# Optimization experiments

Measured on AMD Instinct MI355X. Metric: run time of the kernel, lower is better.

Reference implementation:

```python
import jax, jax.numpy as jnp
import numpy as np

NH = 16   # num_heads
HD = 128  # head_dim
HS = 2048 # hidden_size
LI, LT = 2048, 512
MLP = 4 * HS


def _ln(x, s, b):
    m = jnp.mean(x, axis=-1, keepdims=True)
    v = jnp.var(x, axis=-1, keepdims=True)
    return (x - m) * jax.lax.rsqrt(v + 1e-6) * s + b


def _rms(x, s):
    return x * jax.lax.rsqrt(jnp.mean(x * x, axis=-1, keepdims=True) + 1e-6) * s


def _mod6(vec, w, b):
    a = (jax.nn.silu(vec) @ w + b)[:, None, :]
    return jnp.split(a, 6, axis=-1)  # shift1,scale1,gate1,shift2,scale2,gate2


def _rope(x, pe):
    B, H, L, D = x.shape
    xr = x.reshape(B, H, L, D // 2, 1, 2)
    return (pe[..., 0] * xr[..., 0] + pe[..., 1] * xr[..., 1]).reshape(B, H, L, D)


def _attention(q, k, v, pe):
    q = _rope(q, pe)
    k = _rope(k, pe)
    scores = jnp.einsum('bhqd,bhkd->bhqk', q, k) * (q.shape[-1] ** -0.5)
    p = jax.nn.softmax(scores, axis=-1)
    o = jnp.einsum('bhqk,bhkd->bhqd', p, v)
    B, H, L, D = o.shape
    return o.transpose(0, 2, 1, 3).reshape(B, L, H * D)


def _prenorm_qkv(x, shift, scale, ln_s, ln_b, qkv_w, qkv_b, qn, kn):
    xm = (1.0 + scale) * _ln(x, ln_s, ln_b) + shift
    y = xm @ qkv_w + qkv_b
    B, L, _ = y.shape
    y = y.reshape(B, L, 3, NH, HD).transpose(2, 0, 3, 1, 4)  # K B H L D
    q, k, v = y[0], y[1], y[2]
    return _rms(q, qn), _rms(k, kn), v


def _forward(img, txt, vec, pe,
             img_mod_w, img_mod_b, img_norm1_s, img_norm1_b, img_qkv_w, img_qkv_b,
             img_qn_s, img_kn_s, img_proj_w, img_proj_b, img_norm2_s, img_norm2_b,
             img_mlp_w1, img_mlp_b1, img_mlp_w2, img_mlp_b2,
             txt_mod_w, txt_mod_b, txt_norm1_s, txt_norm1_b, txt_qkv_w, txt_qkv_b,
             txt_qn_s, txt_kn_s, txt_proj_w, txt_proj_b, txt_norm2_s, txt_norm2_b,
             txt_mlp_w1, txt_mlp_b1, txt_mlp_w2, txt_mlp_b2):
    i_sh1, i_sc1, i_g1, i_sh2, i_sc2, i_g2 = _mod6(vec, img_mod_w, img_mod_b)
    t_sh1, t_sc1, t_g1, t_sh2, t_sc2, t_g2 = _mod6(vec, txt_mod_w, txt_mod_b)

    iq, ik, iv = _prenorm_qkv(img, i_sh1, i_sc1, img_norm1_s, img_norm1_b,
                              img_qkv_w, img_qkv_b, img_qn_s, img_kn_s)
    tq, tk, tv = _prenorm_qkv(txt, t_sh1, t_sc1, txt_norm1_s, txt_norm1_b,
                              txt_qkv_w, txt_qkv_b, txt_qn_s, txt_kn_s)

    q = jnp.concatenate((tq, iq), axis=2)
    k = jnp.concatenate((tk, ik), axis=2)
    v = jnp.concatenate((tv, iv), axis=2)
    attn = _attention(q, k, v, pe)  # [B, LT+LI, HS]
    Lt = txt.shape[1]
    txt_attn, img_attn = attn[:, :Lt], attn[:, Lt:]

    img = img + i_g1 * (img_attn @ img_proj_w + img_proj_b)
    img_h = (1.0 + i_sc2) * _ln(img, img_norm2_s, img_norm2_b) + i_sh2
    img = img + i_g2 * (jax.nn.gelu(img_h @ img_mlp_w1 + img_mlp_b1) @ img_mlp_w2 + img_mlp_b2)

    txt = txt + t_g1 * (txt_attn @ txt_proj_w + txt_proj_b)
    txt_h = (1.0 + t_sc2) * _ln(txt, txt_norm2_s, txt_norm2_b) + t_sh2
    txt = txt + t_g2 * (jax.nn.gelu(txt_h @ txt_mlp_w1 + txt_mlp_b1) @ txt_mlp_w2 + txt_mlp_b2)
    return img, txt


def setup_inputs() -> dict:
    key = jax.random.key(0)
    ki = iter(jax.random.split(key, 48))
    def n(shape, s=0.02):
        return jax.random.normal(next(ki), shape, jnp.float32) * s
    d = {
        'img': jax.random.normal(next(ki), (1, LI, HS), jnp.float32),
        'txt': jax.random.normal(next(ki), (1, LT, HS), jnp.float32),
        'vec': jax.random.normal(next(ki), (1, HS), jnp.float32),
        'pe': jax.random.normal(next(ki), (1, 1, LT + LI, HD // 2, 2, 2), jnp.float32),
    }
    for p in ('img', 'txt'):
        d[p + '_mod_w'] = n((HS, 6 * HS)); d[p + '_mod_b'] = jnp.zeros((6 * HS,), jnp.float32)
        d[p + '_norm1_s'] = jnp.ones((HS,), jnp.float32); d[p + '_norm1_b'] = jnp.zeros((HS,), jnp.float32)
        d[p + '_qkv_w'] = n((HS, 3 * HS)); d[p + '_qkv_b'] = jnp.zeros((3 * HS,), jnp.float32)
        d[p + '_qn_s'] = jnp.ones((HD,), jnp.float32); d[p + '_kn_s'] = jnp.ones((HD,), jnp.float32)
        d[p + '_proj_w'] = n((HS, HS)); d[p + '_proj_b'] = jnp.zeros((HS,), jnp.float32)
        d[p + '_norm2_s'] = jnp.ones((HS,), jnp.float32); d[p + '_norm2_b'] = jnp.zeros((HS,), jnp.float32)
        d[p + '_mlp_w1'] = n((HS, MLP)); d[p + '_mlp_b1'] = jnp.zeros((MLP,), jnp.float32)
        d[p + '_mlp_w2'] = n((MLP, HS)); d[p + '_mlp_b2'] = jnp.zeros((HS,), jnp.float32)
    return d


def reference(img, txt, vec, pe,
              img_mod_w, img_mod_b, img_norm1_s, img_norm1_b, img_qkv_w, img_qkv_b,
              img_qn_s, img_kn_s, img_proj_w, img_proj_b, img_norm2_s, img_norm2_b,
              img_mlp_w1, img_mlp_b1, img_mlp_w2, img_mlp_b2,
              txt_mod_w, txt_mod_b, txt_norm1_s, txt_norm1_b, txt_qkv_w, txt_qkv_b,
              txt_qn_s, txt_kn_s, txt_proj_w, txt_proj_b, txt_norm2_s, txt_norm2_b,
              txt_mlp_w1, txt_mlp_b1, txt_mlp_w2, txt_mlp_b2):
    return _forward(img, txt, vec, pe,
                    img_mod_w, img_mod_b, img_norm1_s, img_norm1_b, img_qkv_w, img_qkv_b,
                    img_qn_s, img_kn_s, img_proj_w, img_proj_b, img_norm2_s, img_norm2_b,
                    img_mlp_w1, img_mlp_b1, img_mlp_w2, img_mlp_b2,
                    txt_mod_w, txt_mod_b, txt_norm1_s, txt_norm1_b, txt_qkv_w, txt_qkv_b,
                    txt_qn_s, txt_kn_s, txt_proj_w, txt_proj_b, txt_norm2_s, txt_norm2_b,
                    txt_mlp_w1, txt_mlp_b1, txt_mlp_w2, txt_mlp_b2)
```

## Files before the change

kernel.cpp:

```cpp
#include <hip/hip_runtime.h>
#include <hip/hip_bf16.h>
#include <math.h>

typedef __bf16 bf16;
typedef __bf16 bf16x2 __attribute__((ext_vector_type(2)));
typedef __bf16 bf16x4 __attribute__((ext_vector_type(4)));
typedef __bf16 bf16x8 __attribute__((ext_vector_type(8)));
typedef float f32x4 __attribute__((ext_vector_type(4)));

#define HS 2048
#define NH 16
#define HD 128
#define LT 512
#define LI 2048
#define LQ 2560
#define MLP_D 8192
#define SPLIT 4
#define KVS (LQ / SPLIT)
#define KVBLK 32
#define NTILES (KVS / KVBLK)

__device__ __forceinline__ f32x4 mfma16(bf16x8 a, bf16x8 b, f32x4 c) {
  return __builtin_amdgcn_mfma_f32_16x16x32_bf16(a, b, c, 0, 0, 0);
}

__device__ __forceinline__ void gl_lds16(const bf16* g, bf16* l) {
  __builtin_amdgcn_global_load_lds((const __attribute__((address_space(1))) void*)g,
                                   (__attribute__((address_space(3))) void*)l, 16, 0, 0);
}

__global__ void k_silu(const float* __restrict__ v, float* __restrict__ s) {
  int i = blockIdx.x * 256 + threadIdx.x;
  float x = v[i];
  s[i] = x / (1.f + expf(-x));
}

__global__ __launch_bounds__(256) void k_mod_partial(
    const float* __restrict__ s, const float* __restrict__ w_txt,
    const float* __restrict__ w_img, float* __restrict__ part) {
  int strm = blockIdx.x / 48;
  int n = (blockIdx.x % 48) * 256 + threadIdx.x;
  const float* w = strm ? w_img : w_txt;
  int k0 = blockIdx.y * 256;
  __shared__ float sl[256];
  sl[threadIdx.x] = s[k0 + threadIdx.x];
  __syncthreads();
  float acc = 0.f;
  for (int k = 0; k < 256; k++)
    acc += sl[k] * w[(size_t)(k0 + k) * 12288 + n];
  part[((size_t)blockIdx.y * 2 + strm) * 12288 + n] = acc;
}

__global__ __launch_bounds__(256) void k_mod_reduce(
    const float* __restrict__ part, const float* __restrict__ b_txt,
    const float* __restrict__ b_img, float* __restrict__ mod) {
  int strm = blockIdx.x / 48;
  int n = (blockIdx.x % 48) * 256 + threadIdx.x;
  float acc = strm ? b_img[n] : b_txt[n];
  for (int kc = 0; kc < 8; kc++)
    acc += part[((size_t)kc * 2 + strm) * 12288 + n];
  mod[(size_t)strm * 12288 + n] = acc;
}

__global__ __launch_bounds__(256) void k_transpose_cvt(
    const float* __restrict__ src, bf16* __restrict__ dst, int R, int C) {
  __shared__ float t[64][65];
  int tx = threadIdx.x & 63, ty = threadIdx.x >> 6;
  int c0 = blockIdx.x * 64, r0 = blockIdx.y * 64;
  for (int i = 0; i < 64; i += 4)
    t[ty + i][tx] = src[(size_t)(r0 + ty + i) * C + c0 + tx];
  __syncthreads();
#pragma unroll
  for (int j = 0; j < 2; j++) {
    int c = (threadIdx.x >> 3) + j * 32;
    int gg = (threadIdx.x & 7) * 8;
    bf16x8 ov;
#pragma unroll
    for (int k = 0; k < 8; k++) ov[k] = (bf16)t[gg + k][c];
    *(bf16x8*)(dst + (size_t)(c0 + c) * R + r0 + gg) = ov;
  }
}

__global__ __launch_bounds__(256) void k_ln_mod(
    const float* __restrict__ x0, const float* __restrict__ x1,
    const float* __restrict__ ls0, const float* __restrict__ lb0,
    const float* __restrict__ ls1, const float* __restrict__ lb1,
    const float* __restrict__ mod0, const float* __restrict__ mod1,
    int shidx, int scidx, bf16* __restrict__ out) {
  int r = blockIdx.x;
  int strm = r >= LT;
  const float* x = strm ? (x1 + (size_t)(r - LT) * HS) : (x0 + (size_t)r * HS);
  const float* ls = strm ? ls1 : ls0;
  const float* lb = strm ? lb1 : lb0;
  const float* md = strm ? mod1 : mod0;
  const float* sh = md + (size_t)shidx * HS;
  const float* sc = md + (size_t)scidx * HS;
  int t = threadIdx.x;
  float4 a = ((const float4*)x)[t * 2];
  float4 b = ((const float4*)x)[t * 2 + 1];
  float xv[8] = {a.x, a.y, a.z, a.w, b.x, b.y, b.z, b.w};
  float sum = 0.f, sq = 0.f;
#pragma unroll
  for (int j = 0; j < 8; j++) { sum += xv[j]; sq += xv[j] * xv[j]; }
#pragma unroll
  for (int m = 32; m; m >>= 1) { sum += __shfl_xor(sum, m); sq += __shfl_xor(sq, m); }
  __shared__ float red[8];
  int lane = t & 63, wid = t >> 6;
  if (!lane) { red[wid] = sum; red[wid + 4] = sq; }
  __syncthreads();
  float ts = red[0] + red[1] + red[2] + red[3];
  float tq = red[4] + red[5] + red[6] + red[7];
  float mean = ts * (1.f / HS);
  float var = tq * (1.f / HS) - mean * mean;
  float inv = rsqrtf(var + 1e-6f);
  int c0 = t * 8;
  bf16x8 ov;
#pragma unroll
  for (int j = 0; j < 8; j++) {
    int c = c0 + j;
    float v = ((xv[j] - mean) * inv * ls[c] + lb[c]) * (1.f + sc[c]) + sh[c];
    ov[j] = (bf16)v;
  }
  *(bf16x8*)(out + (size_t)r * HS + c0) = ov;
}

template <int MODE>
__global__ __launch_bounds__(512, 2) void k_gemm256(
    const bf16* __restrict__ A, int K, int N, int Ksz,
    const bf16* __restrict__ BT0, const bf16* __restrict__ BT1,
    const float* __restrict__ bias0, const float* __restrict__ bias1,
    void* __restrict__ out0, void* __restrict__ out1) {
  __shared__ bf16 As[2][128 * 64];
  __shared__ bf16 Bs[2][256 * 64];
  int tid = threadIdx.x;
  int bn = blockIdx.x, bm = blockIdx.y;
  int strm = (bm * 128) >= LT;
  int lm = bm * 128 - strm * LT;
  const bf16* BT = strm ? BT1 : BT0;
  int lane = tid & 63, wid = tid >> 6;
  int wr = wid >> 2, wc = wid & 3;
  int srow = tid >> 3;
  int col8 = (((tid & 7) ^ (srow & 7)) << 3);
  const bf16* Ag = A + (size_t)(bm * 128 + srow) * K + col8;
  const bf16* Bg = BT + (size_t)(bn * 256 + srow) * K + col8;
  int kbeg = MODE == 4 ? blockIdx.z * Ksz : 0;
  int nk = Ksz / 64;
  auto stage = [&](int buf, int kt) {
    int k0 = kbeg + kt * 64;
#pragma unroll
    for (int j = 0; j < 2; j++)
      gl_lds16(Ag + (size_t)(j * 64) * K + k0, &As[buf][j * 4096 + tid * 8]);
#pragma unroll
    for (int j = 0; j < 4; j++)
      gl_lds16(Bg + (size_t)(j * 64) * K + k0, &Bs[buf][j * 4096 + tid * 8]);
  };
  f32x4 acc[4][4] = {};
  int r16 = lane & 15, g = lane >> 4;
  int sa = r16 & 7;
  stage(0, 0);
  int cur = 0;
  for (int kt = 0; kt < nk; kt++) {
    __syncthreads();
    if (kt + 1 < nk) stage(cur ^ 1, kt + 1);
    bf16x8 af[4][2], bfr[4][2];
#pragma unroll
    for (int m = 0; m < 4; m++) {
      int ar = wr * 64 + m * 16 + r16;
#pragma unroll
      for (int kk = 0; kk < 2; kk++)
        af[m][kk] = *(const bf16x8*)&As[cur][ar * 64 + (((kk * 4 + g) ^ sa) << 3)];
    }
#pragma unroll
    for (int n = 0; n < 4; n++) {
      int br = wc * 64 + n * 16 + r16;
#pragma unroll
      for (int kk = 0; kk < 2; kk++)
        bfr[n][kk] = *(const bf16x8*)&Bs[cur][br * 64 + (((kk * 4 + g) ^ sa) << 3)];
    }
#pragma unroll
    for (int kk = 0; kk < 2; kk++)
#pragma unroll
      for (int m = 0; m < 4; m++)
#pragma unroll
        for (int n = 0; n < 4; n++)
          acc[m][n] = mfma16(af[m][kk], bfr[n][kk], acc[m][n]);
    cur ^= 1;
  }
  int col = lane & 15, rb = (lane >> 4) * 4;
  const float* bias = strm ? bias1 : bias0;
  float* part = MODE == 4 ? (float*)out0 + (size_t)blockIdx.z * LQ * N : nullptr;
#pragma unroll
  for (int m = 0; m < 4; m++) {
#pragma unroll
    for (int n = 0; n < 4; n++) {
      int gn = bn * 256 + wc * 64 + n * 16 + col;
      float bv = MODE == 4 ? 0.f : bias[gn];
#pragma unroll
      for (int r = 0; r < 4; r++) {
        int lr = wr * 64 + m * 16 + rb + r;
        float v = acc[m][n][r] + bv;
        if (MODE == 0) {
          ((bf16*)(strm ? out1 : out0))[(size_t)(lm + lr) * N + gn] = (bf16)v;
        } else if (MODE == 2) {
          float u2 = 1.5957691216057308f * (v + 0.044715f * v * v * v);
          float ge = v / (1.f + __expf(-u2));
          ((bf16*)(strm ? out1 : out0))[(size_t)(lm + lr) * N + gn] = (bf16)ge;
        } else {
          part[(size_t)(bm * 128 + lr) * N + gn] = v;
        }
      }
    }
  }
}

template <int MODE>
__global__ __launch_bounds__(256) void k_gemm(
    const bf16* __restrict__ A, int K, int N, int Ksz,
    const bf16* __restrict__ BT0, const bf16* __restrict__ BT1,
    const float* __restrict__ bias0, const float* __restrict__ bias1,
    void* __restrict__ out0, void* __restrict__ out1) {
  __shared__ bf16 As[2][128 * 32];
  __shared__ bf16 Bs[2][128 * 32];
  int tid = threadIdx.x;
  int bn = blockIdx.x, bm = blockIdx.y;
  int strm = (bm * 128) >= LT;
  int lm = bm * 128 - strm * LT;
  const bf16* BT = strm ? BT1 : BT0;
  int lane = tid & 63, wid = tid >> 6;
  int wr = wid >> 1, wc = wid & 1;
  int sr = tid >> 2;
  int scol = ((tid & 3) ^ (sr & 3)) * 8;
  const bf16* Ag = A + (size_t)(bm * 128 + sr) * K + scol;
  const bf16* Bg = BT + (size_t)(bn * 128 + sr) * K + scol;
  int kbeg = MODE == 4 ? blockIdx.z * Ksz : 0;
  int nk = Ksz / 32;
  auto stage = [&](int buf, int ks) {
    int k0 = kbeg + ks * 32;
    gl_lds16(Ag + k0, &As[buf][wid * 512]);
    gl_lds16(Ag + (size_t)64 * K + k0, &As[buf][2048 + wid * 512]);
    gl_lds16(Bg + k0, &Bs[buf][wid * 512]);
    gl_lds16(Bg + (size_t)64 * K + k0, &Bs[buf][2048 + wid * 512]);
  };
  f32x4 acc[4][4] = {};
  int r16 = lane & 15, g = lane >> 4;
  int fslot = (g ^ (r16 & 3)) * 8;
  stage(0, 0);
  int cur = 0;
  for (int ks = 0; ks < nk; ks++) {
    __syncthreads();
    if (ks + 1 < nk) stage(cur ^ 1, ks + 1);
    bf16x8 af[4], bfr[4];
#pragma unroll
    for (int m = 0; m < 4; m++)
      af[m] = *(const bf16x8*)&As[cur][(wr * 64 + m * 16 + r16) * 32 + fslot];
#pragma unroll
    for (int n = 0; n < 4; n++)
      bfr[n] = *(const bf16x8*)&Bs[cur][(wc * 64 + n * 16 + r16) * 32 + fslot];
#pragma unroll
    for (int m = 0; m < 4; m++)
#pragma unroll
      for (int n = 0; n < 4; n++)
        acc[m][n] = mfma16(af[m], bfr[n], acc[m][n]);
    cur ^= 1;
  }
  int col = lane & 15, rb = (lane >> 4) * 4;
  float* part = (float*)out0 + (size_t)blockIdx.z * LQ * N;
#pragma unroll
  for (int m = 0; m < 4; m++) {
#pragma unroll
    for (int n = 0; n < 4; n++) {
      int gn = bn * 128 + wc * 64 + n * 16 + col;
#pragma unroll
      for (int r = 0; r < 4; r++) {
        int lr = wr * 64 + m * 16 + rb + r;
        part[(size_t)(bm * 128 + lr) * N + gn] = acc[m][n][r];
      }
    }
  }
  (void)bias0; (void)bias1; (void)out1; (void)lm;
}

template <int S>
__global__ __launch_bounds__(256) void k_skcomb(
    const float* __restrict__ part, int N,
    const float* __restrict__ bias0, const float* __restrict__ bias1,
    const float* __restrict__ gate0, const float* __restrict__ gate1,
    const float* __restrict__ res0, const float* __restrict__ res1,
    float* __restrict__ out0, float* __restrict__ out1) {
  int gid = blockIdx.x * 256 + threadIdx.x;
  int nv = N >> 2;
  int row = gid / nv, cv = gid - row * nv;
  int strm = row >= LT;
  int lrow = row - strm * LT;
  const float* bias = strm ? bias1 : bias0;
  const float* gate = strm ? gate1 : gate0;
  const float* res = strm ? res1 : res0;
  float* out = strm ? out1 : out0;
  int c = cv * 4;
  float4 acc = *(const float4*)(bias + c);
#pragma unroll
  for (int s = 0; s < S; s++) {
    float4 p = *(const float4*)(part + ((size_t)s * LQ + row) * N + c);
    acc.x += p.x; acc.y += p.y; acc.z += p.z; acc.w += p.w;
  }
  float4 g = *(const float4*)(gate + c);
  float4 r = *(const float4*)(res + (size_t)lrow * N + c);
  float4 o = {r.x + g.x * acc.x, r.y + g.y * acc.y, r.z + g.z * acc.z, r.w + g.w * acc.w};
  *(float4*)(out + (size_t)lrow * N + c) = o;
}

__global__ __launch_bounds__(256) void k_qkv_post(
    const bf16* __restrict__ y, const float* __restrict__ pe,
    const float* __restrict__ qn0, const float* __restrict__ kn0,
    const float* __restrict__ qn1, const float* __restrict__ kn1,
    bf16* __restrict__ qh, bf16* __restrict__ kh) {
  int wv = (int)((blockIdx.x * 256 + threadIdx.x) >> 6);
  int lane = threadIdx.x & 63;
  int head = wv / LQ, l = wv - head * LQ;
  const bf16* yr = y + (size_t)l * (3 * HS) + head * HD;
  float q0 = (float)yr[2 * lane], q1 = (float)yr[2 * lane + 1];
  float k0 = (float)yr[HS + 2 * lane], k1 = (float)yr[HS + 2 * lane + 1];
  float sqs = q0 * q0 + q1 * q1, sks = k0 * k0 + k1 * k1;
#pragma unroll
  for (int m = 1; m < 64; m <<= 1) { sqs += __shfl_xor(sqs, m); sks += __shfl_xor(sks, m); }
  float rq = rsqrtf(sqs * (1.f / HD) + 1e-6f);
  float rk = rsqrtf(sks * (1.f / HD) + 1e-6f);
  int strm = l >= LT;
  const float* qn = strm ? qn1 : qn0;
  const float* kn = strm ? kn1 : kn0;
  float e0 = q0 * rq * qn[2 * lane], e1 = q1 * rq * qn[2 * lane + 1];
  float f0 = k0 * rk * kn[2 * lane], f1 = k1 * rk * kn[2 * lane + 1];
  float4 p = *(const float4*)(pe + ((size_t)l * 64 + lane) * 4);
  const float scl = 0.12751744f;
  size_t qi = ((size_t)head * LQ + l) * HD + 2 * lane;
  bf16x2 qv = {(bf16)((p.x * e0 + p.y * e1) * scl), (bf16)((p.z * e0 + p.w * e1) * scl)};
  bf16x2 kv = {(bf16)(p.x * f0 + p.y * f1), (bf16)(p.z * f0 + p.w * f1)};
  *(bf16x2*)(qh + qi) = qv;
  *(bf16x2*)(kh + qi) = kv;
}

__global__ __launch_bounds__(256) void k_vtrans(const bf16* __restrict__ y,
                                                bf16* __restrict__ vT) {
  __shared__ bf16 t[32][34];
  int head = blockIdx.y >> 2, dt = blockIdx.y & 3;
  int tx = threadIdx.x & 31, ty = threadIdx.x >> 5;
  int l0 = blockIdx.x * 32, d0 = dt * 32;
  for (int i = 0; i < 32; i += 8)
    t[ty + i][tx] = y[(size_t)(l0 + ty + i) * (3 * HS) + 2 * HS + head * HD + d0 + tx];
  __syncthreads();
  for (int i = 0; i < 32; i += 8)
    vT[(size_t)(head * HD + d0 + ty + i) * LQ + l0 + tx] = t[tx][ty + i];
}

__global__ __launch_bounds__(256, 5) void k_attn(
    const bf16* __restrict__ Q, const bf16* __restrict__ Kh,
    const bf16* __restrict__ VT, bf16* __restrict__ Op, float* __restrict__ ml) {
  __shared__ bf16 Ks[2][KVBLK * 128];
  __shared__ bf16 Vs[2][128 * KVBLK];
  int tid = threadIdx.x, lane = tid & 63, w = tid >> 6;
  int b = blockIdx.x;
  int qb = b % 40;
  int split = (b / 40) % SPLIT;
  int head = b / (40 * SPLIT);
  int qr = qb * 64 + w * 16;
  int r16 = lane & 15, g = lane >> 4;
  const bf16* qp = Q + ((size_t)head * LQ + qr + r16) * HD + g * 8;
  bf16x8 qf[4];
#pragma unroll
  for (int c = 0; c < 4; c++) qf[c] = *(const bf16x8*)(qp + c * 32);
  f32x4 O[8] = {};
  float mr = -1e30f, lr = 0.f;
  const bf16* kbase = Kh + ((size_t)head * LQ + split * KVS) * HD;
  const bf16* vbase = VT + (size_t)head * HD * LQ + split * KVS;
  int krow0 = w * 8 + (lane >> 4);
  int kslot = lane & 15;
  int vrow0 = w * 32 + (lane >> 2);
  int vslot = lane & 3;
  auto stage = [&](int buf, int t) {
    int kv0 = t * KVBLK;
#pragma unroll
    for (int i = 0; i < 2; i++) {
      int krow = krow0 + i * 4;
      gl_lds16(kbase + (size_t)(kv0 + krow) * HD + ((kslot ^ (krow & 7)) << 3),
               &Ks[buf][(w * 8 + i * 4) * 128]);
      int vrow = vrow0 + i * 16;
      gl_lds16(vbase + (size_t)vrow * LQ + kv0 + ((vslot ^ (vrow & 3)) << 3),
               &Vs[buf][(w * 32 + i * 16) * KVBLK]);
    }
  };
  stage(0, 0);
  int cur = 0;
  int src0 = r16 + ((g & 1) << 5);
  bool hiS = g >= 2;
  for (int t = 0; t < NTILES; t++) {
    __syncthreads();
    if (t + 1 < NTILES) stage(cur ^ 1, t + 1);
    const bf16* ks = &Ks[cur][0];
    const bf16* vs = &Vs[cur][0];
    f32x4 S0 = {}, S1 = {};
    int sw = (r16 & 7);
#pragma unroll
    for (int c = 0; c < 4; c++) {
      int slot = ((4 * c + g) ^ sw) << 3;
      bf16x8 ka = *(const bf16x8*)&ks[r16 * 128 + slot];
      bf16x8 kb = *(const bf16x8*)&ks[(16 + r16) * 128 + slot];
      S0 = mfma16(ka, qf[c], S0);
      S1 = mfma16(kb, qf[c], S1);
    }
    float mx = fmaxf(fmaxf(fmaxf(S0[0], S0[1]), fmaxf(S0[2], S0[3])),
                     fmaxf(fmaxf(S1[0], S1[1]), fmaxf(S1[2], S1[3])));
    mx = fmaxf(mx, __shfl_xor(mx, 16));
    mx = fmaxf(mx, __shfl_xor(mx, 32));
    bool keep = __all(mx <= mr + 8.f);
    float alpha = 1.f;
    if (!keep) {
      float mn = fmaxf(mr, mx);
      alpha = exp2f(mr - mn);
      mr = mn;
    }
    float p0 = exp2f(S0[0] - mr), p1 = exp2f(S0[1] - mr);
    float p2 = exp2f(S0[2] - mr), p3 = exp2f(S0[3] - mr);
    float p4 = exp2f(S1[0] - mr), p5 = exp2f(S1[1] - mr);
    float p6 = exp2f(S1[2] - mr), p7 = exp2f(S1[3] - mr);
    float rs = ((p0 + p1) + (p2 + p3)) + ((p4 + p5) + (p6 + p7));
    rs += __shfl_xor(rs, 16);
    rs += __shfl_xor(rs, 32);
    lr = fmaf(lr, alpha, rs);
    bf16x2 a0 = {(bf16)p0, (bf16)p1}, a1 = {(bf16)p2, (bf16)p3};
    bf16x2 b0 = {(bf16)p4, (bf16)p5}, b1 = {(bf16)p6, (bf16)p7};
    int A0 = *(int*)&a0, A1 = *(int*)&a1, B0 = *(int*)&b0, B1 = *(int*)&b1;
    int x0a = __shfl(A0, src0), x0b = __shfl(B0, src0);
    int x1a = __shfl(A1, src0), x1b = __shfl(B1, src0);
    int x2a = __shfl(A0, src0 + 16), x2b = __shfl(B0, src0 + 16);
    int x3a = __shfl(A1, src0 + 16), x3b = __shfl(B1, src0 + 16);
    union { int u[4]; bf16x8 v; } pu;
    pu.u[0] = hiS ? x0b : x0a;
    pu.u[1] = hiS ? x1b : x1a;
    pu.u[2] = hiS ? x2b : x2a;
    pu.u[3] = hiS ? x3b : x3a;
    bf16x8 pf = pu.v;
    if (!keep) {
#pragma unroll
      for (int n = 0; n < 8; n++) O[n] *= alpha;
    }
    int vsl = (g ^ (r16 & 3)) * 8;
#pragma unroll
    for (int n = 0; n < 8; n++) {
      bf16x8 vf = *(const bf16x8*)&vs[(n * 16 + r16) * KVBLK + vsl];
      O[n] = mfma16(vf, pf, O[n]);
    }
    cur ^= 1;
  }
  const int NL = NH * LQ;
  bf16* op = Op + (size_t)split * NL * HD;
  size_t rowbase = ((size_t)head * LQ + qr + r16) * HD + 4 * g;
#pragma unroll
  for (int n = 0; n < 8; n++) {
    bf16x4 ov = {(bf16)O[n][0], (bf16)O[n][1], (bf16)O[n][2], (bf16)O[n][3]};
    *(bf16x4*)(op + rowbase + n * 16) = ov;
  }
  if (g == 0) {
    int idx = head * LQ + qr + r16;
    ml[(size_t)(split * 2 + 0) * NL + idx] = mr;
    ml[(size_t)(split * 2 + 1) * NL + idx] = lr;
  }
}

__global__ __launch_bounds__(256) void k_attn_combine(
    const bf16* __restrict__ Op, const float* __restrict__ ml, bf16* __restrict__ out) {
  int lane = threadIdx.x & 63, w = threadIdx.x >> 6;
  int row = blockIdx.x * 4 + w;
  int head = row / LQ, l = row - head * LQ;
  const int NL = NH * LQ;
  float ms[SPLIT], ls[SPLIT], m = -1e30f;
#pragma unroll
  for (int s = 0; s < SPLIT; s++) {
    ms[s] = ml[(size_t)(s * 2) * NL + row];
    ls[s] = ml[(size_t)(s * 2 + 1) * NL + row];
    m = fmaxf(m, ms[s]);
  }
  float wsum = 0.f, wgt[SPLIT];
#pragma unroll
  for (int s = 0; s < SPLIT; s++) { wgt[s] = exp2f(ms[s] - m); wsum += wgt[s] * ls[s]; }
  float inv = 1.f / wsum;
  size_t oi = (size_t)row * HD + 2 * lane;
  float a0 = 0.f, a1 = 0.f;
#pragma unroll
  for (int s = 0; s < SPLIT; s++) {
    bf16x2 v = *(const bf16x2*)(Op + (size_t)s * NL * HD + oi);
    a0 += wgt[s] * (float)v[0];
    a1 += wgt[s] * (float)v[1];
  }
  bf16x2 ov = {(bf16)(a0 * inv), (bf16)(a1 * inv)};
  *(bf16x2*)(out + (size_t)l * HS + head * HD + 2 * lane) = ov;
}

extern "C" void kernel_launch(void* const* d_in, const int* in_sizes, int n_in,
                              void* d_out, int out_size, void* d_ws, size_t ws_size,
                              hipStream_t stream) {
  const float* img = (const float*)d_in[0];
  const float* txt = (const float*)d_in[1];
  const float* vec = (const float*)d_in[2];
  const float* pe = (const float*)d_in[3];
#define PARAM(i) ((const float*)d_in[i])

  char* ws = (char*)d_ws;
  size_t off = 0;
  auto alloc = [&](size_t b) { void* p = ws + off; off += (b + 255) & ~(size_t)255; return p; };
  float* silu_s = (float*)alloc((size_t)HS * 4);
  float* mpart = (float*)alloc((size_t)8 * 2 * 12288 * 4);
  float* mod = (float*)alloc((size_t)2 * 6 * HS * 4);
  bf16* qkvT0 = (bf16*)alloc((size_t)3 * HS * HS * 2);
  bf16* qkvT1 = (bf16*)alloc((size_t)3 * HS * HS * 2);
  bf16* projT0 = (bf16*)alloc((size_t)HS * HS * 2);
  bf16* projT1 = (bf16*)alloc((size_t)HS * HS * 2);
  bf16* mlp1T0 = (bf16*)alloc((size_t)MLP_D * HS * 2);
  bf16* mlp1T1 = (bf16*)alloc((size_t)MLP_D * HS * 2);
  bf16* mlp2T0 = (bf16*)alloc((size_t)HS * MLP_D * 2);
  bf16* mlp2T1 = (bf16*)alloc((size_t)HS * MLP_D * 2);
  bf16* xm = (bf16*)alloc((size_t)LQ * HS * 2);
  bf16* y = (bf16*)alloc((size_t)LQ * 3 * HS * 2);
  bf16* qh = (bf16*)alloc((size_t)NH * LQ * HD * 2);
  bf16* kh = (bf16*)alloc((size_t)NH * LQ * HD * 2);
  bf16* vT = (bf16*)alloc((size_t)NH * HD * LQ * 2);
  bf16* attnb = (bf16*)alloc((size_t)LQ * HS * 2);
  float* x2 = (float*)alloc((size_t)LQ * HS * 4);
  bf16* xm2 = (bf16*)alloc((size_t)LQ * HS * 2);
  bf16* h = (bf16*)alloc((size_t)LQ * MLP_D * 2);
  float* ml = (float*)alloc((size_t)2 * SPLIT * NH * LQ * 4);
  bf16* Op = h;
  float* skpart = (float*)xm;
  (void)ws_size; (void)in_sizes; (void)n_in; (void)out_size;

  const float* t_mod = mod;
  const float* i_mod = mod + 6 * HS;

  k_silu<<<HS / 256, 256, 0, stream>>>(vec, silu_s);
  k_mod_partial<<<dim3(96, 8), 256, 0, stream>>>(silu_s, PARAM(20), PARAM(4), mpart);
  k_mod_reduce<<<96, 256, 0, stream>>>(mpart, PARAM(21), PARAM(5), mod);

  k_transpose_cvt<<<dim3(3 * HS / 64, HS / 64), 256, 0, stream>>>(PARAM(24), qkvT0, HS, 3 * HS);
  k_transpose_cvt<<<dim3(3 * HS / 64, HS / 64), 256, 0, stream>>>(PARAM(8), qkvT1, HS, 3 * HS);
  k_transpose_cvt<<<dim3(HS / 64, HS / 64), 256, 0, stream>>>(PARAM(28), projT0, HS, HS);
  k_transpose_cvt<<<dim3(HS / 64, HS / 64), 256, 0, stream>>>(PARAM(12), projT1, HS, HS);
  k_transpose_cvt<<<dim3(MLP_D / 64, HS / 64), 256, 0, stream>>>(PARAM(32), mlp1T0, HS, MLP_D);
  k_transpose_cvt<<<dim3(MLP_D / 64, HS / 64), 256, 0, stream>>>(PARAM(16), mlp1T1, HS, MLP_D);
  k_transpose_cvt<<<dim3(HS / 64, MLP_D / 64), 256, 0, stream>>>(PARAM(34), mlp2T0, MLP_D, HS);
  k_transpose_cvt<<<dim3(HS / 64, MLP_D / 64), 256, 0, stream>>>(PARAM(18), mlp2T1, MLP_D, HS);

  k_ln_mod<<<LQ, 256, 0, stream>>>(txt, img, PARAM(22), PARAM(23), PARAM(6), PARAM(7),
                                   t_mod, i_mod, 0, 1, xm);

  k_gemm256<0><<<dim3(3 * HS / 256, LQ / 128), 512, 0, stream>>>(
      xm, HS, 3 * HS, HS, qkvT0, qkvT1, PARAM(25), PARAM(9), y, y + (size_t)LT * 3 * HS);

  k_qkv_post<<<NH * LQ / 4, 256, 0, stream>>>(y, pe, PARAM(26), PARAM(27), PARAM(10), PARAM(11),
                                              qh, kh);
  k_vtrans<<<dim3(LQ / 32, NH * 4), 256, 0, stream>>>(y, vT);

  k_attn<<<NH * SPLIT * 40, 256, 0, stream>>>(qh, kh, vT, Op, ml);
  k_attn_combine<<<NH * LQ / 4, 256, 0, stream>>>(Op, ml, attnb);

  k_gemm<4><<<dim3(HS / 128, LQ / 128, 2), 256, 0, stream>>>(
      attnb, HS, HS, HS / 2, projT0, projT1, nullptr, nullptr, skpart, nullptr);
  k_skcomb<2><<<LQ * HS / 4 / 256, 256, 0, stream>>>(
      skpart, HS, PARAM(29), PARAM(13), t_mod + 2 * HS, i_mod + 2 * HS, txt, img,
      x2, x2 + (size_t)LT * HS);

  k_ln_mod<<<LQ, 256, 0, stream>>>(x2, x2 + (size_t)LT * HS, PARAM(30), PARAM(31), PARAM(14),
                                   PARAM(15), t_mod, i_mod, 3, 4, xm2);

  k_gemm256<2><<<dim3(MLP_D / 256, LQ / 128), 512, 0, stream>>>(
      xm2, HS, MLP_D, HS, mlp1T0, mlp1T1, PARAM(33), PARAM(17), h, h + (size_t)LT * MLP_D);

  float* out_img = (float*)d_out;
  float* out_txt = (float*)d_out + (size_t)LI * HS;
  k_gemm256<4><<<dim3(HS / 256, LQ / 128, 4), 512, 0, stream>>>(
      h, MLP_D, HS, MLP_D / 4, mlp2T0, mlp2T1, nullptr, nullptr, skpart, nullptr);
  k_skcomb<4><<<LQ * HS / 4 / 256, 256, 0, stream>>>(
      skpart, HS, PARAM(35), PARAM(19), t_mod + 5 * HS, i_mod + 5 * HS, x2,
      x2 + (size_t)LT * HS, out_txt, out_img);
}
```

Measured before the change: 814.5 us.

## Replace 128x256 GEMM with 256x256 eight-phase pipelined kernel with interleaved prefetch

```diff
diff --git a/kernel.cpp b/kernel.cpp
--- a/kernel.cpp
+++ b/kernel.cpp
@@ -125,80 +125,150 @@
 }
 
 template <int MODE>
-__global__ __launch_bounds__(512, 2) void k_gemm256(
+__global__ __launch_bounds__(512, 2) void k_gemm8p(
     const bf16* __restrict__ A, int K, int N, int Ksz,
     const bf16* __restrict__ BT0, const bf16* __restrict__ BT1,
     const float* __restrict__ bias0, const float* __restrict__ bias1,
     void* __restrict__ out0, void* __restrict__ out1) {
-  __shared__ bf16 As[2][128 * 64];
+  __shared__ bf16 As[2][256 * 64];
   __shared__ bf16 Bs[2][256 * 64];
   int tid = threadIdx.x;
   int bn = blockIdx.x, bm = blockIdx.y;
-  int strm = (bm * 128) >= LT;
-  int lm = bm * 128 - strm * LT;
+  int strm = (bm * 256) >= LT;
+  int lm = bm * 256 - strm * LT;
   const bf16* BT = strm ? BT1 : BT0;
   int lane = tid & 63, wid = tid >> 6;
   int wr = wid >> 2, wc = wid & 3;
   int srow = tid >> 3;
-  int col8 = (((tid & 7) ^ (srow & 7)) << 3);
-  const bf16* Ag = A + (size_t)(bm * 128 + srow) * K + col8;
-  const bf16* Bg = BT + (size_t)(bn * 256 + srow) * K + col8;
+  int scol = (((tid & 7) ^ (srow & 7)) << 3);
+  const bf16* Ag = A + (size_t)(bm * 256 + srow) * K + scol;
+  const bf16* Bg = BT + (size_t)(bn * 256 + srow) * K + scol;
   int kbeg = MODE == 4 ? blockIdx.z * Ksz : 0;
-  int nk = Ksz / 64;
-  auto stage = [&](int buf, int kt) {
-    int k0 = kbeg + kt * 64;
+  int NT = Ksz / 64;
+  auto stageA = [&](int b, int tt, int h) {
+    int k0 = kbeg + tt * 64;
 #pragma unroll
     for (int j = 0; j < 2; j++)
-      gl_lds16(Ag + (size_t)(j * 64) * K + k0, &As[buf][j * 4096 + tid * 8]);
-#pragma unroll
-    for (int j = 0; j < 4; j++)
-      gl_lds16(Bg + (size_t)(j * 64) * K + k0, &Bs[buf][j * 4096 + tid * 8]);
+      gl_lds16(Ag + (size_t)(h * 128 + j * 64) * K + k0,
+               &As[b][(h * 128 + j * 64) * 64 + tid * 8]);
   };
-  f32x4 acc[4][4] = {};
+  auto stageB = [&](int b, int tt, int h) {
+    int k0 = kbeg + tt * 64;
+#pragma unroll
+    for (int j = 0; j < 2; j++)
+      gl_lds16(Bg + (size_t)(h * 128 + j * 64) * K + k0,
+               &Bs[b][(h * 128 + j * 64) * 64 + tid * 8]);
+  };
+  f32x4 acc[8][4] = {};
   int r16 = lane & 15, g = lane >> 4;
   int sa = r16 & 7;
-  stage(0, 0);
-  int cur = 0;
-  for (int kt = 0; kt < nk; kt++) {
-    __syncthreads();
-    if (kt + 1 < nk) stage(cur ^ 1, kt + 1);
-    bf16x8 af[4][2], bfr[4][2];
+  stageA(0, 0, 0); stageA(0, 0, 1); stageB(0, 0, 0); stageB(0, 0, 1);
+  if (NT > 1) stageA(1, 1, 0);
+  bf16x8 Ar[4][2], Br[2][2][2];
+  for (int t = 0; t < NT; t++) {
+    int c = t & 1;
+    const bf16* as = &As[c][0];
+    const bf16* bs = &Bs[c][0];
+    bool pf1 = (t + 1 < NT);
+    if (pf1) stageA(c ^ 1, t + 1, 1);
+    if (pf1) asm volatile("s_waitcnt vmcnt(4)" ::: "memory");
+    else     asm volatile("s_waitcnt vmcnt(0)" ::: "memory");
 #pragma unroll
     for (int m = 0; m < 4; m++) {
-      int ar = wr * 64 + m * 16 + r16;
+      int ar = wr * 128 + m * 16 + r16;
 #pragma unroll
       for (int kk = 0; kk < 2; kk++)
-        af[m][kk] = *(const bf16x8*)&As[cur][ar * 64 + (((kk * 4 + g) ^ sa) << 3)];
-    }
-#pragma unroll
-    for (int n = 0; n < 4; n++) {
+        Ar[m][kk] = *(const bf16x8*)&as[ar * 64 + (((kk * 4 + g) ^ sa) << 3)];
+    }
+#pragma unroll
+    for (int n = 0; n < 2; n++) {
       int br = wc * 64 + n * 16 + r16;
 #pragma unroll
       for (int kk = 0; kk < 2; kk++)
-        bfr[n][kk] = *(const bf16x8*)&Bs[cur][br * 64 + (((kk * 4 + g) ^ sa) << 3)];
-    }
+        Br[0][n][kk] = *(const bf16x8*)&bs[br * 64 + (((kk * 4 + g) ^ sa) << 3)];
+    }
+    __builtin_amdgcn_s_barrier();
+    asm volatile("s_waitcnt lgkmcnt(0)" ::: "memory");
+    __builtin_amdgcn_sched_barrier(0);
+    __builtin_amdgcn_s_setprio(1);
 #pragma unroll
     for (int kk = 0; kk < 2; kk++)
 #pragma unroll
       for (int m = 0; m < 4; m++)
 #pragma unroll
-        for (int n = 0; n < 4; n++)
-          acc[m][n] = mfma16(af[m][kk], bfr[n][kk], acc[m][n]);
-    cur ^= 1;
-  }
-  int col = lane & 15, rb = (lane >> 4) * 4;
+        for (int n = 0; n < 2; n++)
+          acc[m][n] = mfma16(Ar[m][kk], Br[0][n][kk], acc[m][n]);
+    __builtin_amdgcn_s_setprio(0);
+    __builtin_amdgcn_s_barrier();
+    if (pf1) stageB(c ^ 1, t + 1, 0);
+#pragma unroll
+    for (int n = 0; n < 2; n++) {
+      int br = wc * 64 + 32 + n * 16 + r16;
+#pragma unroll
+      for (int kk = 0; kk < 2; kk++)
+        Br[1][n][kk] = *(const bf16x8*)&bs[br * 64 + (((kk * 4 + g) ^ sa) << 3)];
+    }
+    __builtin_amdgcn_s_barrier();
+    asm volatile("s_waitcnt lgkmcnt(0)" ::: "memory");
+    __builtin_amdgcn_sched_barrier(0);
+    __builtin_amdgcn_s_setprio(1);
+#pragma unroll
+    for (int kk = 0; kk < 2; kk++)
+#pragma unroll
+      for (int m = 0; m < 4; m++)
+#pragma unroll
+        for (int n = 0; n < 2; n++)
+          acc[m][2 + n] = mfma16(Ar[m][kk], Br[1][n][kk], acc[m][2 + n]);
+    __builtin_amdgcn_s_setprio(0);
+    __builtin_amdgcn_s_barrier();
+    if (pf1) stageB(c ^ 1, t + 1, 1);
+#pragma unroll
+    for (int m = 0; m < 4; m++) {
+      int ar = wr * 128 + 64 + m * 16 + r16;
+#pragma unroll
+      for (int kk = 0; kk < 2; kk++)
+        Ar[m][kk] = *(const bf16x8*)&as[ar * 64 + (((kk * 4 + g) ^ sa) << 3)];
+    }
+    __builtin_amdgcn_s_barrier();
+    asm volatile("s_waitcnt lgkmcnt(0)" ::: "memory");
+    __builtin_amdgcn_sched_barrier(0);
+    __builtin_amdgcn_s_setprio(1);
+#pragma unroll
+    for (int kk = 0; kk < 2; kk++)
+#pragma unroll
+      for (int m = 0; m < 4; m++)
+#pragma unroll
+        for (int n = 0; n < 2; n++)
+          acc[4 + m][n] = mfma16(Ar[m][kk], Br[0][n][kk], acc[4 + m][n]);
+    __builtin_amdgcn_s_setprio(0);
+    __builtin_amdgcn_s_barrier();
+    if (t + 2 < NT) stageA(c, t + 2, 0);
+    __builtin_amdgcn_s_barrier();
+    __builtin_amdgcn_s_setprio(1);
+#pragma unroll
+    for (int kk = 0; kk < 2; kk++)
+#pragma unroll
+      for (int m = 0; m < 4; m++)
+#pragma unroll
+        for (int n = 0; n < 2; n++)
+          acc[4 + m][2 + n] = mfma16(Ar[m][kk], Br[1][n][kk], acc[4 + m][2 + n]);
+    __builtin_amdgcn_s_setprio(0);
+    __builtin_amdgcn_s_barrier();
+  }
+  int col = lane & 15, rb = g * 4;
   const float* bias = strm ? bias1 : bias0;
-  float* part = MODE == 4 ? (float*)out0 + (size_t)blockIdx.z * LQ * N : nullptr;
-#pragma unroll
-  for (int m = 0; m < 4; m++) {
-#pragma unroll
-    for (int n = 0; n < 4; n++) {
-      int gn = bn * 256 + wc * 64 + n * 16 + col;
+  float* part = (MODE == 4) ? (float*)out0 + (size_t)blockIdx.z * LQ * N : nullptr;
+#pragma unroll
+  for (int qm = 0; qm < 8; qm++) {
+    int lr0 = wr * 128 + (qm >> 2) * 64 + (qm & 3) * 16 + rb;
+#pragma unroll
+    for (int hn = 0; hn < 4; hn++) {
+      int gn = bn * 256 + wc * 64 + (hn >> 1) * 32 + (hn & 1) * 16 + col;
       float bv = MODE == 4 ? 0.f : bias[gn];
 #pragma unroll
       for (int r = 0; r < 4; r++) {
-        int lr = wr * 64 + m * 16 + rb + r;
-        float v = acc[m][n][r] + bv;
+        int lr = lr0 + r;
+        float v = acc[qm][hn][r] + bv;
         if (MODE == 0) {
           ((bf16*)(strm ? out1 : out0))[(size_t)(lm + lr) * N + gn] = (bf16)v;
         } else if (MODE == 2) {
@@ -206,7 +276,7 @@
           float ge = v / (1.f + __expf(-u2));
           ((bf16*)(strm ? out1 : out0))[(size_t)(lm + lr) * N + gn] = (bf16)ge;
         } else {
-          part[(size_t)(bm * 128 + lr) * N + gn] = v;
+          part[(size_t)(bm * 256 + lr) * N + gn] = v;
         }
       }
     }
@@ -232,7 +302,7 @@
   int scol = ((tid & 3) ^ (sr & 3)) * 8;
   const bf16* Ag = A + (size_t)(bm * 128 + sr) * K + scol;
   const bf16* Bg = BT + (size_t)(bn * 128 + sr) * K + scol;
-  int kbeg = MODE == 4 ? blockIdx.z * Ksz : 0;
+  int kbeg = blockIdx.z * Ksz;
   int nk = Ksz / 32;
   auto stage = [&](int buf, int ks) {
     int k0 = kbeg + ks * 32;
@@ -551,7 +621,7 @@
   k_ln_mod<<<LQ, 256, 0, stream>>>(txt, img, PARAM(22), PARAM(23), PARAM(6), PARAM(7),
                                    t_mod, i_mod, 0, 1, xm);
 
-  k_gemm256<0><<<dim3(3 * HS / 256, LQ / 128), 512, 0, stream>>>(
+  k_gemm8p<0><<<dim3(3 * HS / 256, LQ / 256), 512, 0, stream>>>(
       xm, HS, 3 * HS, HS, qkvT0, qkvT1, PARAM(25), PARAM(9), y, y + (size_t)LT * 3 * HS);
 
   k_qkv_post<<<NH * LQ / 4, 256, 0, stream>>>(y, pe, PARAM(26), PARAM(27), PARAM(10), PARAM(11),
@@ -570,14 +640,14 @@
   k_ln_mod<<<LQ, 256, 0, stream>>>(x2, x2 + (size_t)LT * HS, PARAM(30), PARAM(31), PARAM(14),
                                    PARAM(15), t_mod, i_mod, 3, 4, xm2);
 
-  k_gemm256<2><<<dim3(MLP_D / 256, LQ / 128), 512, 0, stream>>>(
+  k_gemm8p<2><<<dim3(MLP_D / 256, LQ / 256), 512, 0, stream>>>(
       xm2, HS, MLP_D, HS, mlp1T0, mlp1T1, PARAM(33), PARAM(17), h, h + (size_t)LT * MLP_D);
 
   float* out_img = (float*)d_out;
   float* out_txt = (float*)d_out + (size_t)LI * HS;
-  k_gemm256<4><<<dim3(HS / 256, LQ / 128, 4), 512, 0, stream>>>(
-      h, MLP_D, HS, MLP_D / 4, mlp2T0, mlp2T1, nullptr, nullptr, skpart, nullptr);
-  k_skcomb<4><<<LQ * HS / 4 / 256, 256, 0, stream>>>(
+  k_gemm8p<4><<<dim3(HS / 256, LQ / 256, 2), 512, 0, stream>>>(
+      h, MLP_D, HS, MLP_D / 2, mlp2T0, mlp2T1, nullptr, nullptr, skpart, nullptr);
+  k_skcomb<2><<<LQ * HS / 4 / 256, 256, 0, stream>>>(
       skpart, HS, PARAM(35), PARAM(19), t_mod + 5 * HS, i_mod + 5 * HS, x2,
       x2 + (size_t)LT * HS, out_txt, out_img);
 }
```

After: 930.7 us. 14.3% more time.
